# Optimization experiments

Measured on AMD Instinct MI355X. Metric: run time of the kernel, lower is better.

## Reference

```python
import jax, jax.numpy as jnp
import numpy as np

N = 50000      # nodes
E = 800000     # edges (before self loops)
F_IN = 128     # input feature dim
H = 4          # attention heads
C = 64         # per-head channels (hidden_dim = out_channels = 64)
HC = H * C     # 256, concat output width of each GATv2Conv
G = 32         # number of graphs in the batch
NEG_SLOPE_ATT = 0.2   # GATv2 internal LeakyReLU
NEG_SLOPE_ACT = 0.01  # encoder nn.LeakyReLU() default


def _glorot(key, shape, fan_in):
    return jax.random.normal(key, shape, jnp.float32) * (1.0 / np.sqrt(fan_in))


def setup_inputs() -> dict:
    key = jax.random.key(0)
    ks = jax.random.split(key, 32)
    inp = {}
    inp["x"] = jax.random.normal(ks[0], (N, F_IN), jnp.float32)
    inp["edge_index"] = jax.random.randint(ks[1], (2, E), 0, N, jnp.int32)
    inp["batch"] = jnp.sort(jax.random.randint(ks[2], (N,), 0, G, jnp.int32))
    i = 3
    for li, fin in ((1, F_IN), (2, HC), (3, HC)):
        inp[f"Wl{li}"] = _glorot(ks[i], (HC, fin), fin); i += 1
        inp[f"bl{li}"] = jnp.zeros((HC,), jnp.float32)
        inp[f"Wr{li}"] = _glorot(ks[i], (HC, fin), fin); i += 1
        inp[f"br{li}"] = jnp.zeros((HC,), jnp.float32)
        inp[f"att{li}"] = _glorot(ks[i], (H, C), C); i += 1
        inp[f"bo{li}"] = jnp.zeros((HC,), jnp.float32)
    return inp


def _gatv2_layer(x, src, dst, Wl, bl, Wr, br, att, bo):
    n = x.shape[0]
    xl = (x @ Wl.T + bl).reshape(n, H, C)  # source transform
    xr = (x @ Wr.T + br).reshape(n, H, C)  # target transform
    # per-edge attention logits: a^T LeakyReLU(xl[j] + xr[i])
    e = jax.nn.leaky_relu(xl[src] + xr[dst], negative_slope=NEG_SLOPE_ATT)  # [E', H, C]
    score = jnp.einsum('ehc,hc->eh', e, att)                                # [E', H]
    # segment softmax over incoming edges of each destination node
    m = jax.ops.segment_max(score, dst, num_segments=n)
    p = jnp.exp(score - m[dst])
    s = jax.ops.segment_sum(p, dst, num_segments=n)
    alpha = p / s[dst]
    out = jax.ops.segment_sum(alpha[:, :, None] * xl[src], dst, num_segments=n)
    return out.reshape(n, HC) + bo


def reference(x, edge_index, batch,
              Wl1, bl1, Wr1, br1, att1, bo1,
              Wl2, bl2, Wr2, br2, att2, bo2,
              Wl3, bl3, Wr3, br3, att3, bo3):
    loop = jnp.arange(N, dtype=edge_index.dtype)
    src = jnp.concatenate([edge_index[0], loop])  # add self loops (PyG default)
    dst = jnp.concatenate([edge_index[1], loop])
    h = _gatv2_layer(x, src, dst, Wl1, bl1, Wr1, br1, att1, bo1)
    h = jax.nn.leaky_relu(h, negative_slope=NEG_SLOPE_ACT)
    h = _gatv2_layer(h, src, dst, Wl2, bl2, Wr2, br2, att2, bo2)
    h = jax.nn.leaky_relu(h, negative_slope=NEG_SLOPE_ACT)
    h = _gatv2_layer(h, src, dst, Wl3, bl3, Wr3, br3, att3, bo3)
    # global mean pool over graphs
    sums = jax.ops.segment_sum(h, batch, num_segments=G)
    cnt = jax.ops.segment_sum(jnp.ones((N,), h.dtype), batch, num_segments=G)
    return sums / jnp.maximum(cnt, 1.0)[:, None]
```

## Files before the change

kernel.cpp:

```cpp
#include <hip/hip_runtime.h>

#define HEADS 4
#define CH 64
#define HC 256
#define NGRAPH 32
#define NEG_ATT 0.2f
#define NEG_ACT 0.01f

typedef __attribute__((ext_vector_type(8))) short bf16x8;
typedef __attribute__((ext_vector_type(4))) float f32x4;
typedef __attribute__((ext_vector_type(2))) float f32x2;

typedef __attribute__((address_space(3))) unsigned int lds_u32;
typedef const __attribute__((address_space(1))) unsigned int glob_u32;

__device__ __forceinline__ void gl_lds16(const void* g, void* l) {
  __builtin_amdgcn_global_load_lds((glob_u32*)(uintptr_t)g,
                                   (lds_u32*)(unsigned int)(uintptr_t)l, 16, 0, 0);
}

__device__ __forceinline__ void split2(float a, float b, unsigned& hi, unsigned& lo) {
  unsigned ua = __float_as_uint(a), ub = __float_as_uint(b);
  float la = a - __uint_as_float(ua & 0xFFFF0000u);
  float lb = b - __uint_as_float(ub & 0xFFFF0000u);
  hi = __builtin_amdgcn_perm(ub, ua, 0x07060302u);
  lo = __builtin_amdgcn_perm(__float_as_uint(lb), __float_as_uint(la), 0x07060302u);
}

__device__ __forceinline__ unsigned rtn_bf16(float f) {
  unsigned u = __float_as_uint(f);
  return (u + 0x7FFFu + ((u >> 16) & 1u)) >> 16;
}

__global__ __launch_bounds__(256) void convert_x(
    const float* __restrict__ X, unsigned short* __restrict__ xhi,
    unsigned short* __restrict__ xlo, int total4) {
  int g = blockIdx.x * 256 + threadIdx.x;
  if (g >= total4) return;
  float4 v = *(const float4*)&X[(size_t)g * 4];
  uint2 h2, l2;
  split2(v.x, v.y, h2.x, l2.x);
  split2(v.z, v.w, h2.y, l2.y);
  *(uint2*)&xhi[(size_t)g * 4] = h2;
  *(uint2*)&xlo[(size_t)g * 4] = l2;
}

__global__ __launch_bounds__(256) void convert_w_frag(
    const float* __restrict__ Wl, const float* __restrict__ Wr,
    unsigned short* __restrict__ wfhi, unsigned short* __restrict__ wflo, int K) {
  int g = blockIdx.x * 256 + threadIdx.x;
  int lane = g & 63;
  int ct = (g >> 6) & 31;
  int kb = g >> 11;
  int col = ct * 16 + (lane & 15);
  int k = kb * 32 + (lane >> 4) * 8;
  const float* src = (col < HC) ? &Wl[(size_t)col * K + k] : &Wr[(size_t)(col - HC) * K + k];
  float4 v0 = *(const float4*)src;
  float4 v1 = *(const float4*)(src + 4);
  uint4 hq, lq;
  split2(v0.x, v0.y, hq.x, lq.x);
  split2(v0.z, v0.w, hq.y, lq.y);
  split2(v1.x, v1.y, hq.z, lq.z);
  split2(v1.z, v1.w, hq.w, lq.w);
  *(uint4*)&wfhi[(size_t)g * 8] = hq;
  *(uint4*)&wflo[(size_t)g * 8] = lq;
}

template <int K>
__global__ __launch_bounds__(256) void gemm_fused(
    const unsigned short* __restrict__ xhi, const unsigned short* __restrict__ xlo,
    const unsigned short* __restrict__ wfhi, const unsigned short* __restrict__ wflo,
    const float* __restrict__ bl, const float* __restrict__ br,
    unsigned short* __restrict__ Y1, float* __restrict__ Y2, int N) {
  constexpr int nkb = K >> 5;
  __shared__ unsigned short Ah[2][128][32];
  __shared__ unsigned short Al[2][128][32];

  const int tid = threadIdx.x;
  const int wave = tid >> 6;
  const int lane = tid & 63;
  const int quad = lane >> 4;
  const int l16 = lane & 15;
  const int wr = (wave >> 1) * 64;
  const int wc = (wave & 1) * 64;
  const int col0 = blockIdx.x * 128;
  const int row0 = blockIdx.y * 128;
  const int ctg0 = blockIdx.x * 8 + (wave & 1) * 4;

  const int c0 = tid, c1 = tid + 256;
  const int r0g = row0 + (c0 >> 2), r1g = row0 + (c1 >> 2);
  const int ko0 = (c0 & 3) * 8, ko1 = (c1 & 3) * 8;
  const int gr0 = (r0g < N) ? r0g : N - 1;
  const int gr1 = (r1g < N) ? r1g : N - 1;

  f32x4 acc[4][4];
#pragma unroll
  for (int i = 0; i < 4; i++)
#pragma unroll
    for (int j = 0; j < 4; j++) acc[i][j] = (f32x4){0.f, 0.f, 0.f, 0.f};

  bf16x8 bhi[2][4], blo[2][4];
#pragma unroll
  for (int j = 0; j < 4; j++) {
    size_t ci = (size_t)(ctg0 + j) * 64 + lane;
    bhi[0][j] = *(const bf16x8*)&wfhi[ci * 8];
    blo[0][j] = *(const bf16x8*)&wflo[ci * 8];
  }
  {
    size_t ga0 = (size_t)gr0 * K + ko0;
    size_t ga1 = (size_t)gr1 * K + ko1;
    gl_lds16(&xhi[ga0], &Ah[0][c0 >> 2][ko0]);
    gl_lds16(&xlo[ga0], &Al[0][c0 >> 2][ko0]);
    gl_lds16(&xhi[ga1], &Ah[0][c1 >> 2][ko1]);
    gl_lds16(&xlo[ga1], &Al[0][c1 >> 2][ko1]);
  }

#pragma unroll
  for (int kb = 0; kb < nkb; kb++) {
    const int cur = kb & 1, nxt = cur ^ 1;
    __syncthreads();
    if (kb + 1 < nkb) {
      int k0 = (kb + 1) * 32;
      size_t ga0 = (size_t)gr0 * K + k0 + ko0;
      size_t ga1 = (size_t)gr1 * K + k0 + ko1;
      gl_lds16(&xhi[ga0], &Ah[nxt][c0 >> 2][ko0]);
      gl_lds16(&xlo[ga0], &Al[nxt][c0 >> 2][ko0]);
      gl_lds16(&xhi[ga1], &Ah[nxt][c1 >> 2][ko1]);
      gl_lds16(&xlo[ga1], &Al[nxt][c1 >> 2][ko1]);
    }
    bf16x8 ahi[4], alo[4];
#pragma unroll
    for (int i = 0; i < 4; i++) {
      ahi[i] = *(const bf16x8*)&Ah[cur][wr + i * 16 + l16][quad * 8];
      alo[i] = *(const bf16x8*)&Al[cur][wr + i * 16 + l16][quad * 8];
    }
    if (kb + 1 < nkb) {
#pragma unroll
      for (int j = 0; j < 4; j++) {
        size_t ci = ((size_t)(kb + 1) * 32 + ctg0 + j) * 64 + lane;
        bhi[nxt][j] = *(const bf16x8*)&wfhi[ci * 8];
        blo[nxt][j] = *(const bf16x8*)&wflo[ci * 8];
      }
    }
#pragma unroll
    for (int i = 0; i < 4; i++)
#pragma unroll
      for (int j = 0; j < 4; j++) {
        acc[i][j] = __builtin_amdgcn_mfma_f32_16x16x32_bf16(ahi[i], bhi[cur][j], acc[i][j], 0, 0, 0);
        acc[i][j] = __builtin_amdgcn_mfma_f32_16x16x32_bf16(ahi[i], blo[cur][j], acc[i][j], 0, 0, 0);
        acc[i][j] = __builtin_amdgcn_mfma_f32_16x16x32_bf16(alo[i], bhi[cur][j], acc[i][j], 0, 0, 0);
      }
  }

#pragma unroll
  for (int j = 0; j < 4; j++) {
    int colg = col0 + wc + j * 16 + l16;
    if (colg < HC) {
      float bv = bl[colg];
#pragma unroll
      for (int i = 0; i < 4; i++)
#pragma unroll
        for (int r = 0; r < 4; r++) {
          int row = row0 + wr + i * 16 + quad * 4 + r;
          if (row < N)
            Y1[(size_t)row * HC + colg] = (unsigned short)rtn_bf16(acc[i][j][r] + bv);
        }
    } else {
      int cc = colg - HC;
      float bv = br[cc];
#pragma unroll
      for (int i = 0; i < 4; i++)
#pragma unroll
        for (int r = 0; r < 4; r++) {
          int row = row0 + wr + i * 16 + quad * 4 + r;
          if (row < N) Y2[(size_t)row * HC + cc] = acc[i][j][r] + bv;
        }
    }
  }
}

__global__ __launch_bounds__(256) void hist_dst(
    const int* __restrict__ edst, int* __restrict__ counts, int E) {
  int e = blockIdx.x * 256 + threadIdx.x;
  if (e < E) atomicAdd(&counts[edst[e]], 1);
}

__global__ __launch_bounds__(256) void scan_blocks(
    const int* __restrict__ counts, int* __restrict__ row_start,
    int* __restrict__ bsum, int N) {
  __shared__ int tmp[256];
  int t = threadIdx.x;
  int base = blockIdx.x * 1024 + t * 4;
  int v0 = (base     < N) ? counts[base]     + 1 : 0;
  int v1 = (base + 1 < N) ? counts[base + 1] + 1 : 0;
  int v2 = (base + 2 < N) ? counts[base + 2] + 1 : 0;
  int v3 = (base + 3 < N) ? counts[base + 3] + 1 : 0;
  int c1 = v0 + v1, c2 = c1 + v2, tot = c2 + v3;
  tmp[t] = tot;
  __syncthreads();
  for (int off = 1; off < 256; off <<= 1) {
    int add = (t >= off) ? tmp[t - off] : 0;
    __syncthreads();
    tmp[t] += add;
    __syncthreads();
  }
  int excl = tmp[t] - tot;
  if (base     < N) row_start[base + 1] = excl + v0;
  if (base + 1 < N) row_start[base + 2] = excl + c1;
  if (base + 2 < N) row_start[base + 3] = excl + c2;
  if (base + 3 < N) row_start[base + 4] = excl + tot;
  if (t == 255) bsum[blockIdx.x] = tmp[255];
  if (blockIdx.x == 0 && t == 0) row_start[0] = 0;
}

__global__ void scan_tops(int* __restrict__ bsum, int nb) {
  int lane = threadIdx.x;
  int v = (lane < nb) ? bsum[lane] : 0;
  for (int off = 1; off < 64; off <<= 1) {
    int u = __shfl_up(v, off);
    if (lane >= off) v += u;
  }
  if (lane < nb) bsum[lane] = v;
}

__global__ __launch_bounds__(256) void scan_add(
    int* __restrict__ row_start, const int* __restrict__ bsum, int N) {
  int off = bsum[blockIdx.x];
  int i = (blockIdx.x + 1) * 1024 + threadIdx.x * 4;
#pragma unroll
  for (int k = 0; k < 4; k++)
    if (i + k < N) row_start[i + k + 1] += off;
}

__global__ __launch_bounds__(256) void csr_init(
    const int* __restrict__ row_start, int* __restrict__ fill_pos,
    int* __restrict__ csr_src, int N) {
  int i = blockIdx.x * 256 + threadIdx.x;
  if (i < N) {
    int p = row_start[i];
    csr_src[p] = i << 9;
    fill_pos[i] = p + 1;
  }
}

__global__ __launch_bounds__(256) void csr_scatter(
    const int* __restrict__ esrc, const int* __restrict__ edst,
    int* __restrict__ fill_pos, int* __restrict__ csr_src, int E) {
  int e = blockIdx.x * 256 + threadIdx.x;
  if (e < E) {
    int p = atomicAdd(&fill_pos[edst[e]], 1);
    csr_src[p] = esrc[e] << 9;
  }
}

__device__ __forceinline__ void unpk(uint2 q, f32x2& v01, f32x2& v23) {
  v01.x = __uint_as_float(q.x << 16);
  v01.y = __uint_as_float(q.x & 0xFFFF0000u);
  v23.x = __uint_as_float(q.y << 16);
  v23.y = __uint_as_float(q.y & 0xFFFF0000u);
}

__device__ __forceinline__ float edot(f32x2 l01, f32x2 l23, f32x2 r01, f32x2 r23,
                                      f32x2 a01, f32x2 a23) {
  f32x2 t01 = l01 + r01, t23 = l23 + r23;
  f32x2 u01 = t01 * NEG_ATT, u23 = t23 * NEG_ATT;
  t01.x = fmaxf(t01.x, u01.x); t01.y = fmaxf(t01.y, u01.y);
  t23.x = fmaxf(t23.x, u23.x); t23.y = fmaxf(t23.y, u23.y);
  f32x2 dv = t01 * a01 + t23 * a23;
  float d = dv.x + dv.y;
  d += __shfl_xor(d, 1);
  d += __shfl_xor(d, 2);
  d += __shfl_xor(d, 4);
  d += __shfl_xor(d, 8);
  return d;
}

__global__ __launch_bounds__(256) void gat_fused(
    const unsigned short* __restrict__ xl, const float* __restrict__ xr,
    const int* __restrict__ row_start, const int* __restrict__ csr_soff,
    const float* __restrict__ att, const float* __restrict__ bo,
    float* __restrict__ outf, unsigned short* __restrict__ ohi,
    unsigned short* __restrict__ olo, int N, int split_out) {
  int dst = (blockIdx.x * 256 + threadIdx.x) >> 6;
  int lane = threadIdx.x & 63;
  if (dst >= N) return;
  int h = lane >> 4;
  int off = h * CH + (lane & 15) * 4;
  const int loff = off * 2;
  const char* xlc = (const char*)xl;
  f32x2 a01 = *(const f32x2*)&att[off];
  f32x2 a23 = *(const f32x2*)&att[off + 2];
  f32x2 r01 = *(const f32x2*)&xr[(size_t)dst * HC + off];
  f32x2 r23 = *(const f32x2*)&xr[(size_t)dst * HC + off + 2];
  f32x2 o01 = {0.f, 0.f}, o23 = {0.f, 0.f};
  float m = -__builtin_inff();
  float s = 0.f;
  int p = row_start[dst];
  int end = row_start[dst + 1];
  for (; p + 4 <= end; p += 4) {
    int b0 = csr_soff[p + 0] + loff, b1 = csr_soff[p + 1] + loff;
    int b2 = csr_soff[p + 2] + loff, b3 = csr_soff[p + 3] + loff;
    uint2 q0 = *(const uint2*)(xlc + b0);
    uint2 q1 = *(const uint2*)(xlc + b1);
    uint2 q2 = *(const uint2*)(xlc + b2);
    uint2 q3 = *(const uint2*)(xlc + b3);
    f32x2 l0a, l0b, l1a, l1b, l2a, l2b, l3a, l3b;
    unpk(q0, l0a, l0b);
    unpk(q1, l1a, l1b);
    unpk(q2, l2a, l2b);
    unpk(q3, l3a, l3b);
    float d0 = edot(l0a, l0b, r01, r23, a01, a23);
    float d1 = edot(l1a, l1b, r01, r23, a01, a23);
    float d2 = edot(l2a, l2b, r01, r23, a01, a23);
    float d3 = edot(l3a, l3b, r01, r23, a01, a23);
    float newm = fmaxf(fmaxf(fmaxf(d0, d1), fmaxf(d2, d3)), m);
    float sc = __expf(m - newm);
    float e0 = __expf(d0 - newm), e1 = __expf(d1 - newm);
    float e2 = __expf(d2 - newm), e3 = __expf(d3 - newm);
    s = fmaf(s, sc, (e0 + e1) + (e2 + e3));
    f32x2 acc01 = l0a * e0 + l1a * e1;
    acc01 = l2a * e2 + acc01;
    acc01 = l3a * e3 + acc01;
    o01 = o01 * sc + acc01;
    f32x2 acc23 = l0b * e0 + l1b * e1;
    acc23 = l2b * e2 + acc23;
    acc23 = l3b * e3 + acc23;
    o23 = o23 * sc + acc23;
    m = newm;
  }
  for (; p < end; p++) {
    int b0 = csr_soff[p] + loff;
    uint2 q0 = *(const uint2*)(xlc + b0);
    f32x2 la, lb;
    unpk(q0, la, lb);
    float d = edot(la, lb, r01, r23, a01, a23);
    float newm = fmaxf(m, d);
    float sc = __expf(m - newm);
    float pe = __expf(d - newm);
    s = fmaf(s, sc, pe);
    o01 = o01 * sc + la * pe;
    o23 = o23 * sc + lb * pe;
    m = newm;
  }
  float inv = 1.f / s;
  f32x2 b01 = *(const f32x2*)&bo[off];
  f32x2 b23 = *(const f32x2*)&bo[off + 2];
  f32x2 res01 = o01 * inv + b01;
  f32x2 res23 = o23 * inv + b23;
  if (split_out) {
    f32x2 v01 = res01 * NEG_ACT, v23 = res23 * NEG_ACT;
    res01.x = fmaxf(res01.x, v01.x); res01.y = fmaxf(res01.y, v01.y);
    res23.x = fmaxf(res23.x, v23.x); res23.y = fmaxf(res23.y, v23.y);
    uint2 h2, l2;
    split2(res01.x, res01.y, h2.x, l2.x);
    split2(res23.x, res23.y, h2.y, l2.y);
    *(uint2*)&ohi[(size_t)dst * HC + off] = h2;
    *(uint2*)&olo[(size_t)dst * HC + off] = l2;
  } else {
    float4 r4 = {res01.x, res01.y, res23.x, res23.y};
    *(float4*)&outf[(size_t)dst * HC + off] = r4;
  }
}

__global__ __launch_bounds__(256) void pool_partial(
    const float* __restrict__ h, const int* __restrict__ batch,
    float* __restrict__ out, int* __restrict__ cnt, int N) {
  __shared__ float part[NGRAPH][HC];
  __shared__ int bsh[256];
  __shared__ int cpart[NGRAPH];
  int j = threadIdx.x;
#pragma unroll
  for (int g = 0; g < NGRAPH; g++) part[g][j] = 0.f;
  if (j < NGRAPH) cpart[j] = 0;
  int n0 = blockIdx.x * 256;
  int nend = min(n0 + 256, N);
  int nj = n0 + j;
  bsh[j] = (nj < N) ? batch[nj] : 0;
  __syncthreads();
  if (nj < nend) atomicAdd(&cpart[bsh[j]], 1);
  for (int n = n0; n < nend; n++) {
    int g = bsh[n - n0];
    part[g][j] += h[(size_t)n * HC + j];
  }
  __syncthreads();
#pragma unroll
  for (int g = 0; g < NGRAPH; g++) {
    float v = part[g][j];
    if (v != 0.f) atomicAdd(&out[g * HC + j], v);
  }
  if (j < NGRAPH && cpart[j] > 0) atomicAdd(&cnt[j], cpart[j]);
}

__global__ __launch_bounds__(256) void pool_final(
    float* __restrict__ out, const int* __restrict__ cnt) {
  int g = blockIdx.x;
  int j = threadIdx.x;
  float c = (float)max(cnt[g], 1);
  out[g * HC + j] /= c;
}

extern "C" void kernel_launch(void* const* d_in, const int* in_sizes, int n_in,
                              void* d_out, int out_size, void* d_ws, size_t ws_size,
                              hipStream_t stream) {
  const float* x = (const float*)d_in[0];
  const int* ei = (const int*)d_in[1];
  const int* batch = (const int*)d_in[2];
  const int N = in_sizes[2];
  const int E = in_sizes[1] / 2;
  const int Etot = E + N;

  const float* Wl[3] = {(const float*)d_in[3], (const float*)d_in[9], (const float*)d_in[15]};
  const float* bl[3] = {(const float*)d_in[4], (const float*)d_in[10], (const float*)d_in[16]};
  const float* Wr[3] = {(const float*)d_in[5], (const float*)d_in[11], (const float*)d_in[17]};
  const float* br[3] = {(const float*)d_in[6], (const float*)d_in[12], (const float*)d_in[18]};
  const float* att[3] = {(const float*)d_in[7], (const float*)d_in[13], (const float*)d_in[19]};
  const float* bo[3] = {(const float*)d_in[8], (const float*)d_in[14], (const float*)d_in[20]};

  float* B0 = (float*)d_ws;
  float* B1 = B0 + (size_t)N * HC;
  float* B2 = B1 + (size_t)N * HC;
  unsigned short* w1hi = (unsigned short*)(B2 + (size_t)N * HC);
  unsigned short* w1lo = w1hi + 512 * 128;
  unsigned short* w2hi = w1lo + 512 * 128;
  unsigned short* w2lo = w2hi + 512 * 256;
  unsigned short* w3hi = w2lo + 512 * 256;
  unsigned short* w3lo = w3hi + 512 * 256;
  int* counts = (int*)(w3lo + 512 * 256);
  int* row_start = counts + N;
  int* bsum = row_start + N + 1;
  int* fill_pos = bsum + 64;
  int* csr_src = fill_pos + N;
  int* cnt = csr_src + Etot;

  unsigned short* xlB = (unsigned short*)B1;
  unsigned short* xhiL1 = (unsigned short*)B0;
  unsigned short* xloL1 = xhiL1 + (size_t)N * 128;
  unsigned short* xhiL = (unsigned short*)B0;
  unsigned short* xloL = xhiL + (size_t)N * HC;

  const int* esrc = ei;
  const int* edst = ei + E;

  convert_x<<<(N * 128 / 4 + 255) / 256, 256, 0, stream>>>(x, xhiL1, xloL1, N * 128 / 4);
  convert_w_frag<<<128 * 64 / 256, 256, 0, stream>>>(Wl[0], Wr[0], w1hi, w1lo, 128);
  convert_w_frag<<<256 * 64 / 256, 256, 0, stream>>>(Wl[1], Wr[1], w2hi, w2lo, 256);
  convert_w_frag<<<256 * 64 / 256, 256, 0, stream>>>(Wl[2], Wr[2], w3hi, w3lo, 256);

  const int nscan = (N + 1023) / 1024;
  (void)hipMemsetAsync(counts, 0, (size_t)N * sizeof(int), stream);
  hist_dst<<<(E + 255) / 256, 256, 0, stream>>>(edst, counts, E);
  scan_blocks<<<nscan, 256, 0, stream>>>(counts, row_start, bsum, N);
  scan_tops<<<1, 64, 0, stream>>>(bsum, nscan);
  scan_add<<<nscan - 1, 256, 0, stream>>>(row_start, bsum, N);
  csr_init<<<(N + 255) / 256, 256, 0, stream>>>(row_start, fill_pos, csr_src, N);
  csr_scatter<<<(E + 255) / 256, 256, 0, stream>>>(esrc, edst, fill_pos, csr_src, E);

  const dim3 ggrid(4, (N + 127) / 128);
  const int fblocks = (N * 64 + 255) / 256;

  gemm_fused<128><<<ggrid, 256, 0, stream>>>(xhiL1, xloL1, w1hi, w1lo, bl[0], br[0], xlB, B2, N);
  gat_fused<<<fblocks, 256, 0, stream>>>(xlB, B2, row_start, csr_src, att[0], bo[0],
                                         nullptr, xhiL, xloL, N, 1);
  gemm_fused<256><<<ggrid, 256, 0, stream>>>(xhiL, xloL, w2hi, w2lo, bl[1], br[1], xlB, B2, N);
  gat_fused<<<fblocks, 256, 0, stream>>>(xlB, B2, row_start, csr_src, att[1], bo[1],
                                         nullptr, xhiL, xloL, N, 1);
  gemm_fused<256><<<ggrid, 256, 0, stream>>>(xhiL, xloL, w3hi, w3lo, bl[2], br[2], xlB, B2, N);
  gat_fused<<<fblocks, 256, 0, stream>>>(xlB, B2, row_start, csr_src, att[2], bo[2],
                                         B0, nullptr, nullptr, N, 0);

  (void)hipMemsetAsync(d_out, 0, NGRAPH * HC * sizeof(float), stream);
  (void)hipMemsetAsync(cnt, 0, NGRAPH * sizeof(int), stream);
  pool_partial<<<(N + 255) / 256, 256, 0, stream>>>(B0, batch, (float*)d_out, cnt, N);
  pool_final<<<NGRAPH, 256, 0, stream>>>((float*)d_out, cnt);
}
```

Baseline: 692.1 us.

## Store xr and final layer output in bf16, drop online-max softmax, direct pooling

Stores the target transform xr and the last-layer output as bf16 instead of fp32, which cuts memory traffic in the GEMM epilogue, the gather kernel and pooling. The online-max softmax rescaling in gat_fused is removed, so raw exponentials are accumulated; this risks overflow when logits are large. Several other changes come with it. The three weight conversions merge into one launch. GEMM blocks are remapped to a swizzled 1D grid that groups row blocks for L2 reuse, and the B-fragment prefetch register double-buffer is removed. The atomic pooling plus final-divide kernels are replaced by a per-graph kernel that binary-searches the sorted batch vector.

```diff
diff --git a/kernel.cpp b/kernel.cpp
--- a/kernel.cpp
+++ b/kernel.cpp
@@ -30,6 +30,9 @@
 __device__ __forceinline__ unsigned rtn_bf16(float f) {
   unsigned u = __float_as_uint(f);
   return (u + 0x7FFFu + ((u >> 16) & 1u)) >> 16;
+}
+__device__ __forceinline__ unsigned rtn_pack2(float a, float b) {
+  return (rtn_bf16(b) << 16) | rtn_bf16(a);
 }
 
 __global__ __launch_bounds__(256) void convert_x(
@@ -45,10 +48,9 @@
   *(uint2*)&xlo[(size_t)g * 4] = l2;
 }
 
-__global__ __launch_bounds__(256) void convert_w_frag(
-    const float* __restrict__ Wl, const float* __restrict__ Wr,
-    unsigned short* __restrict__ wfhi, unsigned short* __restrict__ wflo, int K) {
-  int g = blockIdx.x * 256 + threadIdx.x;
+__device__ __forceinline__ void conv_w_one(
+    int g, const float* Wl, const float* Wr, int K,
+    unsigned short* wfhi, unsigned short* wflo) {
   int lane = g & 63;
   int ct = (g >> 6) & 31;
   int kb = g >> 11;
@@ -66,15 +68,33 @@
   *(uint4*)&wflo[(size_t)g * 8] = lq;
 }
 
+__global__ __launch_bounds__(256) void convert_w_all(
+    const float* __restrict__ Wl1, const float* __restrict__ Wr1,
+    unsigned short* __restrict__ w1hi, unsigned short* __restrict__ w1lo,
+    const float* __restrict__ Wl2, const float* __restrict__ Wr2,
+    unsigned short* __restrict__ w2hi, unsigned short* __restrict__ w2lo,
+    const float* __restrict__ Wl3, const float* __restrict__ Wr3,
+    unsigned short* __restrict__ w3hi, unsigned short* __restrict__ w3lo) {
+  int g = blockIdx.x * 256 + threadIdx.x;
+  if (g < 8192) conv_w_one(g, Wl1, Wr1, 128, w1hi, w1lo);
+  else if (g < 8192 + 16384) conv_w_one(g - 8192, Wl2, Wr2, 256, w2hi, w2lo);
+  else conv_w_one(g - 8192 - 16384, Wl3, Wr3, 256, w3hi, w3lo);
+}
+
 template <int K>
 __global__ __launch_bounds__(256) void gemm_fused(
     const unsigned short* __restrict__ xhi, const unsigned short* __restrict__ xlo,
     const unsigned short* __restrict__ wfhi, const unsigned short* __restrict__ wflo,
     const float* __restrict__ bl, const float* __restrict__ br,
-    unsigned short* __restrict__ Y1, float* __restrict__ Y2, int N) {
+    unsigned short* __restrict__ Y1, unsigned short* __restrict__ Y2, int N, int nrb) {
   constexpr int nkb = K >> 5;
   __shared__ unsigned short Ah[2][128][32];
   __shared__ unsigned short Al[2][128][32];
+
+  const int f = blockIdx.x;
+  const int rb = (f & 7) + 8 * (f >> 5);
+  const int cb = (f >> 3) & 3;
+  if (rb >= nrb) return;
 
   const int tid = threadIdx.x;
   const int wave = tid >> 6;
@@ -83,9 +103,9 @@
   const int l16 = lane & 15;
   const int wr = (wave >> 1) * 64;
   const int wc = (wave & 1) * 64;
-  const int col0 = blockIdx.x * 128;
-  const int row0 = blockIdx.y * 128;
-  const int ctg0 = blockIdx.x * 8 + (wave & 1) * 4;
+  const int row0 = rb * 128;
+  const int col0 = cb * 128;
+  const int ctg0 = cb * 8 + (wave & 1) * 4;
 
   const int c0 = tid, c1 = tid + 256;
   const int r0g = row0 + (c0 >> 2), r1g = row0 + (c1 >> 2);
@@ -99,13 +119,6 @@
 #pragma unroll
     for (int j = 0; j < 4; j++) acc[i][j] = (f32x4){0.f, 0.f, 0.f, 0.f};
 
-  bf16x8 bhi[2][4], blo[2][4];
-#pragma unroll
-  for (int j = 0; j < 4; j++) {
-    size_t ci = (size_t)(ctg0 + j) * 64 + lane;
-    bhi[0][j] = *(const bf16x8*)&wfhi[ci * 8];
-    blo[0][j] = *(const bf16x8*)&wflo[ci * 8];
-  }
   {
     size_t ga0 = (size_t)gr0 * K + ko0;
     size_t ga1 = (size_t)gr1 * K + ko1;
@@ -118,6 +131,13 @@
 #pragma unroll
   for (int kb = 0; kb < nkb; kb++) {
     const int cur = kb & 1, nxt = cur ^ 1;
+    bf16x8 bhi[4], blo[4];
+#pragma unroll
+    for (int j = 0; j < 4; j++) {
+      size_t ci = ((size_t)kb * 32 + ctg0 + j) * 64 + lane;
+      bhi[j] = *(const bf16x8*)&wfhi[ci * 8];
+      blo[j] = *(const bf16x8*)&wflo[ci * 8];
+    }
     __syncthreads();
     if (kb + 1 < nkb) {
       int k0 = (kb + 1) * 32;
@@ -134,48 +154,30 @@
       ahi[i] = *(const bf16x8*)&Ah[cur][wr + i * 16 + l16][quad * 8];
       alo[i] = *(const bf16x8*)&Al[cur][wr + i * 16 + l16][quad * 8];
     }
-    if (kb + 1 < nkb) {
+#pragma unroll
+    for (int i = 0; i < 4; i++)
 #pragma unroll
       for (int j = 0; j < 4; j++) {
-        size_t ci = ((size_t)(kb + 1) * 32 + ctg0 + j) * 64 + lane;
-        bhi[nxt][j] = *(const bf16x8*)&wfhi[ci * 8];
-        blo[nxt][j] = *(const bf16x8*)&wflo[ci * 8];
-      }
-    }
-#pragma unroll
-    for (int i = 0; i < 4; i++)
-#pragma unroll
-      for (int j = 0; j < 4; j++) {
-        acc[i][j] = __builtin_amdgcn_mfma_f32_16x16x32_bf16(ahi[i], bhi[cur][j], acc[i][j], 0, 0, 0);
-        acc[i][j] = __builtin_amdgcn_mfma_f32_16x16x32_bf16(ahi[i], blo[cur][j], acc[i][j], 0, 0, 0);
-        acc[i][j] = __builtin_amdgcn_mfma_f32_16x16x32_bf16(alo[i], bhi[cur][j], acc[i][j], 0, 0, 0);
+        acc[i][j] = __builtin_amdgcn_mfma_f32_16x16x32_bf16(ahi[i], bhi[j], acc[i][j], 0, 0, 0);
+        acc[i][j] = __builtin_amdgcn_mfma_f32_16x16x32_bf16(ahi[i], blo[j], acc[i][j], 0, 0, 0);
+        acc[i][j] = __builtin_amdgcn_mfma_f32_16x16x32_bf16(alo[i], bhi[j], acc[i][j], 0, 0, 0);
       }
   }
 
 #pragma unroll
   for (int j = 0; j < 4; j++) {
     int colg = col0 + wc + j * 16 + l16;
-    if (colg < HC) {
-      float bv = bl[colg];
-#pragma unroll
-      for (int i = 0; i < 4; i++)
-#pragma unroll
-        for (int r = 0; r < 4; r++) {
-          int row = row0 + wr + i * 16 + quad * 4 + r;
-          if (row < N)
-            Y1[(size_t)row * HC + colg] = (unsigned short)rtn_bf16(acc[i][j][r] + bv);
-        }
-    } else {
-      int cc = colg - HC;
-      float bv = br[cc];
-#pragma unroll
-      for (int i = 0; i < 4; i++)
-#pragma unroll
-        for (int r = 0; r < 4; r++) {
-          int row = row0 + wr + i * 16 + quad * 4 + r;
-          if (row < N) Y2[(size_t)row * HC + cc] = acc[i][j][r] + bv;
-        }
-    }
+    unsigned short* Yp = (colg < HC) ? Y1 : Y2;
+    int cc = (colg < HC) ? colg : colg - HC;
+    float bv = (colg < HC) ? bl[cc] : br[cc];
+#pragma unroll
+    for (int i = 0; i < 4; i++)
+#pragma unroll
+      for (int r = 0; r < 4; r++) {
+        int row = row0 + wr + i * 16 + quad * 4 + r;
+        if (row < N)
+          Yp[(size_t)row * HC + cc] = (unsigned short)rtn_bf16(acc[i][j][r] + bv);
+      }
   }
 }
 
@@ -276,11 +278,11 @@
 }
 
 __global__ __launch_bounds__(256) void gat_fused(
-    const unsigned short* __restrict__ xl, const float* __restrict__ xr,
+    const unsigned short* __restrict__ xl, const unsigned short* __restrict__ xr,
     const int* __restrict__ row_start, const int* __restrict__ csr_soff,
     const float* __restrict__ att, const float* __restrict__ bo,
-    float* __restrict__ outf, unsigned short* __restrict__ ohi,
-    unsigned short* __restrict__ olo, int N, int split_out) {
+    unsigned short* __restrict__ ohi, unsigned short* __restrict__ olo,
+    int N, int mode) {
   int dst = (blockIdx.x * 256 + threadIdx.x) >> 6;
   int lane = threadIdx.x & 63;
   if (dst >= N) return;
@@ -290,10 +292,9 @@
   const char* xlc = (const char*)xl;
   f32x2 a01 = *(const f32x2*)&att[off];
   f32x2 a23 = *(const f32x2*)&att[off + 2];
-  f32x2 r01 = *(const f32x2*)&xr[(size_t)dst * HC + off];
-  f32x2 r23 = *(const f32x2*)&xr[(size_t)dst * HC + off + 2];
+  f32x2 r01, r23;
+  unpk(*(const uint2*)&xr[(size_t)dst * HC + off], r01, r23);
   f32x2 o01 = {0.f, 0.f}, o23 = {0.f, 0.f};
-  float m = -__builtin_inff();
   float s = 0.f;
   int p = row_start[dst];
   int end = row_start[dst + 1];
@@ -309,45 +310,36 @@
     unpk(q1, l1a, l1b);
     unpk(q2, l2a, l2b);
     unpk(q3, l3a, l3b);
-    float d0 = edot(l0a, l0b, r01, r23, a01, a23);
-    float d1 = edot(l1a, l1b, r01, r23, a01, a23);
-    float d2 = edot(l2a, l2b, r01, r23, a01, a23);
-    float d3 = edot(l3a, l3b, r01, r23, a01, a23);
-    float newm = fmaxf(fmaxf(fmaxf(d0, d1), fmaxf(d2, d3)), m);
-    float sc = __expf(m - newm);
-    float e0 = __expf(d0 - newm), e1 = __expf(d1 - newm);
-    float e2 = __expf(d2 - newm), e3 = __expf(d3 - newm);
-    s = fmaf(s, sc, (e0 + e1) + (e2 + e3));
-    f32x2 acc01 = l0a * e0 + l1a * e1;
-    acc01 = l2a * e2 + acc01;
-    acc01 = l3a * e3 + acc01;
-    o01 = o01 * sc + acc01;
-    f32x2 acc23 = l0b * e0 + l1b * e1;
-    acc23 = l2b * e2 + acc23;
-    acc23 = l3b * e3 + acc23;
-    o23 = o23 * sc + acc23;
-    m = newm;
+    float e0 = __expf(edot(l0a, l0b, r01, r23, a01, a23));
+    float e1 = __expf(edot(l1a, l1b, r01, r23, a01, a23));
+    float e2 = __expf(edot(l2a, l2b, r01, r23, a01, a23));
+    float e3 = __expf(edot(l3a, l3b, r01, r23, a01, a23));
+    s += (e0 + e1) + (e2 + e3);
+    o01 = l0a * e0 + o01;
+    o01 = l1a * e1 + o01;
+    o01 = l2a * e2 + o01;
+    o01 = l3a * e3 + o01;
+    o23 = l0b * e0 + o23;
+    o23 = l1b * e1 + o23;
+    o23 = l2b * e2 + o23;
+    o23 = l3b * e3 + o23;
   }
   for (; p < end; p++) {
     int b0 = csr_soff[p] + loff;
     uint2 q0 = *(const uint2*)(xlc + b0);
     f32x2 la, lb;
     unpk(q0, la, lb);
-    float d = edot(la, lb, r01, r23, a01, a23);
-    float newm = fmaxf(m, d);
-    float sc = __expf(m - newm);
-    float pe = __expf(d - newm);
-    s = fmaf(s, sc, pe);
-    o01 = o01 * sc + la * pe;
-    o23 = o23 * sc + lb * pe;
-    m = newm;
+    float pe = __expf(edot(la, lb, r01, r23, a01, a23));
+    s += pe;
+    o01 = la * pe + o01;
+    o23 = lb * pe + o23;
   }
   float inv = 1.f / s;
   f32x2 b01 = *(const f32x2*)&bo[off];
   f32x2 b23 = *(const f32x2*)&bo[off + 2];
   f32x2 res01 = o01 * inv + b01;
   f32x2 res23 = o23 * inv + b23;
-  if (split_out) {
+  if (mode == 1) {
     f32x2 v01 = res01 * NEG_ACT, v23 = res23 * NEG_ACT;
     res01.x = fmaxf(res01.x, v01.x); res01.y = fmaxf(res01.y, v01.y);
     res23.x = fmaxf(res23.x, v23.x); res23.y = fmaxf(res23.y, v23.y);
@@ -357,46 +349,43 @@
     *(uint2*)&ohi[(size_t)dst * HC + off] = h2;
     *(uint2*)&olo[(size_t)dst * HC + off] = l2;
   } else {
-    float4 r4 = {res01.x, res01.y, res23.x, res23.y};
-    *(float4*)&outf[(size_t)dst * HC + off] = r4;
-  }
-}
-
-__global__ __launch_bounds__(256) void pool_partial(
-    const float* __restrict__ h, const int* __restrict__ batch,
-    float* __restrict__ out, int* __restrict__ cnt, int N) {
-  __shared__ float part[NGRAPH][HC];
-  __shared__ int bsh[256];
-  __shared__ int cpart[NGRAPH];
-  int j = threadIdx.x;
-#pragma unroll
-  for (int g = 0; g < NGRAPH; g++) part[g][j] = 0.f;
-  if (j < NGRAPH) cpart[j] = 0;
-  int n0 = blockIdx.x * 256;
-  int nend = min(n0 + 256, N);
-  int nj = n0 + j;
-  bsh[j] = (nj < N) ? batch[nj] : 0;
+    uint2 pk;
+    pk.x = rtn_pack2(res01.x, res01.y);
+    pk.y = rtn_pack2(res23.x, res23.y);
+    *(uint2*)&ohi[(size_t)dst * HC + off] = pk;
+  }
+}
+
+__global__ __launch_bounds__(256) void pool_direct(
+    const unsigned short* __restrict__ h3, const int* __restrict__ batch,
+    float* __restrict__ out, int N) {
+  const int g = blockIdx.x;
+  const int t = threadIdx.x;
+  int lo = 0, hi = N;
+  while (lo < hi) { int mid = (lo + hi) >> 1; if (batch[mid] < g) lo = mid + 1; else hi = mid; }
+  int lo2 = lo, hi2 = N;
+  while (lo2 < hi2) { int mid = (lo2 + hi2) >> 1; if (batch[mid] < g + 1) lo2 = mid + 1; else hi2 = mid; }
+  const int cnt = lo2 - lo;
+  const int colu = t & 127;
+  const int rpar = t >> 7;
+  f32x2 acc = {0.f, 0.f};
+  const unsigned* h3u = (const unsigned*)h3;
+  for (int n = lo + rpar; n < lo2; n += 2) {
+    unsigned q = h3u[(size_t)n * 128 + colu];
+    f32x2 v;
+    v.x = __uint_as_float(q << 16);
+    v.y = __uint_as_float(q & 0xFFFF0000u);
+    acc += v;
+  }
+  __shared__ f32x2 sh[2][128];
+  sh[rpar][colu] = acc;
   __syncthreads();
-  if (nj < nend) atomicAdd(&cpart[bsh[j]], 1);
-  for (int n = n0; n < nend; n++) {
-    int g = bsh[n - n0];
-    part[g][j] += h[(size_t)n * HC + j];
-  }
-  __syncthreads();
-#pragma unroll
-  for (int g = 0; g < NGRAPH; g++) {
-    float v = part[g][j];
-    if (v != 0.f) atomicAdd(&out[g * HC + j], v);
-  }
-  if (j < NGRAPH && cpart[j] > 0) atomicAdd(&cnt[j], cpart[j]);
-}
-
-__global__ __launch_bounds__(256) void pool_final(
-    float* __restrict__ out, const int* __restrict__ cnt) {
-  int g = blockIdx.x;
-  int j = threadIdx.x;
-  float c = (float)max(cnt[g], 1);
-  out[g * HC + j] /= c;
+  if (t < 128) {
+    f32x2 tot = sh[0][t] + sh[1][t];
+    float c = (float)max(cnt, 1);
+    f32x2 res = tot * (1.f / c);
+    *(f32x2*)&out[g * HC + t * 2] = res;
+  }
 }
 
 extern "C" void kernel_launch(void* const* d_in, const int* in_sizes, int n_in,
@@ -430,21 +419,21 @@
   int* bsum = row_start + N + 1;
   int* fill_pos = bsum + 64;
   int* csr_src = fill_pos + N;
-  int* cnt = csr_src + Etot;
 
   unsigned short* xlB = (unsigned short*)B1;
+  unsigned short* xrB = (unsigned short*)B2;
   unsigned short* xhiL1 = (unsigned short*)B0;
   unsigned short* xloL1 = xhiL1 + (size_t)N * 128;
   unsigned short* xhiL = (unsigned short*)B0;
   unsigned short* xloL = xhiL + (size_t)N * HC;
+  unsigned short* h3B = (unsigned short*)B0;
 
   const int* esrc = ei;
   const int* edst = ei + E;
 
   convert_x<<<(N * 128 / 4 + 255) / 256, 256, 0, stream>>>(x, xhiL1, xloL1, N * 128 / 4);
-  convert_w_frag<<<128 * 64 / 256, 256, 0, stream>>>(Wl[0], Wr[0], w1hi, w1lo, 128);
-  convert_w_frag<<<256 * 64 / 256, 256, 0, stream>>>(Wl[1], Wr[1], w2hi, w2lo, 256);
-  convert_w_frag<<<256 * 64 / 256, 256, 0, stream>>>(Wl[2], Wr[2], w3hi, w3lo, 256);
+  convert_w_all<<<(8192 + 16384 + 16384) / 256, 256, 0, stream>>>(
+      Wl[0], Wr[0], w1hi, w1lo, Wl[1], Wr[1], w2hi, w2lo, Wl[2], Wr[2], w3hi, w3lo);
 
   const int nscan = (N + 1023) / 1024;
   (void)hipMemsetAsync(counts, 0, (size_t)N * sizeof(int), stream);
@@ -455,21 +444,19 @@
   csr_init<<<(N + 255) / 256, 256, 0, stream>>>(row_start, fill_pos, csr_src, N);
   csr_scatter<<<(E + 255) / 256, 256, 0, stream>>>(esrc, edst, fill_pos, csr_src, E);
 
-  const dim3 ggrid(4, (N + 127) / 128);
+  const int nrb = (N + 127) / 128;
+  const int gblocks = ((nrb + 7) / 8) * 32;
   const int fblocks = (N * 64 + 255) / 256;
 
-  gemm_fused<128><<<ggrid, 256, 0, stream>>>(xhiL1, xloL1, w1hi, w1lo, bl[0], br[0], xlB, B2, N);
-  gat_fused<<<fblocks, 256, 0, stream>>>(xlB, B2, row_start, csr_src, att[0], bo[0],
-                                         nullptr, xhiL, xloL, N, 1);
-  gemm_fused<256><<<ggrid, 256, 0, stream>>>(xhiL, xloL, w2hi, w2lo, bl[1], br[1], xlB, B2, N);
-  gat_fused<<<fblocks, 256, 0, stream>>>(xlB, B2, row_start, csr_src, att[1], bo[1],
-                                         nullptr, xhiL, xloL, N, 1);
-  gemm_fused<256><<<ggrid, 256, 0, stream>>>(xhiL, xloL, w3hi, w3lo, bl[2], br[2], xlB, B2, N);
-  gat_fused<<<fblocks, 256, 0, stream>>>(xlB, B2, row_start, csr_src, att[2], bo[2],
-                                         B0, nullptr, nullptr, N, 0);
-
-  (void)hipMemsetAsync(d_out, 0, NGRAPH * HC * sizeof(float), stream);
-  (void)hipMemsetAsync(cnt, 0, NGRAPH * sizeof(int), stream);
-  pool_partial<<<(N + 255) / 256, 256, 0, stream>>>(B0, batch, (float*)d_out, cnt, N);
-  pool_final<<<NGRAPH, 256, 0, stream>>>((float*)d_out, cnt);
-}
+  gemm_fused<128><<<gblocks, 256, 0, stream>>>(xhiL1, xloL1, w1hi, w1lo, bl[0], br[0], xlB, xrB, N, nrb);
+  gat_fused<<<fblocks, 256, 0, stream>>>(xlB, xrB, row_start, csr_src, att[0], bo[0],
+                                         xhiL, xloL, N, 1);
+  gemm_fused<256><<<gblocks, 256, 0, stream>>>(xhiL, xloL, w2hi, w2lo, bl[1], br[1], xlB, xrB, N, nrb);
+  gat_fused<<<fblocks, 256, 0, stream>>>(xlB, xrB, row_start, csr_src, att[1], bo[1],
+                                         xhiL, xloL, N, 1);
+  gemm_fused<256><<<gblocks, 256, 0, stream>>>(xhiL, xloL, w3hi, w3lo, bl[2], br[2], xlB, xrB, N, nrb);
+  gat_fused<<<fblocks, 256, 0, stream>>>(xlB, xrB, row_start, csr_src, att[2], bo[2],
+                                         h3B, nullptr, N, 2);
+
+  pool_direct<<<NGRAPH, 256, 0, stream>>>(h3B, batch, (float*)d_out, N);
+}
```

Result: slower. 800.7 us (+15.7%).
